# Performance work log

Hardware: AMD Instinct MI355X
Metric: run time of the kernel (lower is better)

## Reference

```python
import jax, jax.numpy as jnp
import numpy as np


def setup_inputs() -> dict:
    key = jax.random.key(0)
    k1, k2, k3 = jax.random.split(key, 3)
    B, C, H, W = 64, 256, 32, 32   # batch, hidden_dim, latent grid
    D, K = 128, 1024               # latent_dim, num_embeddings
    z = jax.random.normal(k1, (B, C, H, W), dtype=jnp.float32)
    proj_w = jax.random.normal(k2, (D, C), dtype=jnp.float32) * 0.02  # 1x1 conv kernel [out,in]
    proj_b = jnp.zeros((D,), jnp.float32)
    # codebook init uniform(-1/K, 1/K) as in torch module
    embed = (jax.random.uniform(k3, (K, D), dtype=jnp.float32) * 2.0 - 1.0) / K
    return {"z": z, "proj_w": proj_w, "proj_b": proj_b, "embed": embed}


def reference(z, proj_w, proj_b, embed):
    # 1x1 conv projection: [B,C,H,W] -> [B,H,W,D]  (fuses conv + permute)
    zp = jnp.einsum('bchw,dc->bhwd', z, proj_w) + proj_b
    B, H, W, D = zp.shape
    zf = zp.reshape(-1, D)                                   # [N, D], N = B*H*W
    # squared Euclidean distance to codebook: ||z||^2 - 2 z.e + ||e||^2  -> [N, K]
    dist = (jnp.sum(zf * zf, axis=1, keepdims=True)
            - 2.0 * (zf @ embed.T)
            + jnp.sum(embed * embed, axis=1))
    min_indices = jnp.argmin(dist, axis=1)                   # [N]
    z_q = embed[min_indices].reshape(B, H, W, D)             # codebook gather
    # straight-through estimator
    rep_z_q = zp + jax.lax.stop_gradient(z_q - zp)
    rep_z_q = rep_z_q.transpose(0, 3, 1, 2)                  # back to NCHW
    return rep_z_q, min_indices
```

## Files before the change

### kernel.cpp

```cpp
#include <hip/hip_runtime.h>

#define B_   64
#define C_   256
#define D_   128
#define HW_  1024
#define K_   1024
#define N_   65536
#define MARGIN_PREF 1.2e-3f

typedef __attribute__((ext_vector_type(8))) short short8;
typedef __attribute__((ext_vector_type(4))) float f32x4;

__device__ __forceinline__ unsigned short f2bf(float f) {
    unsigned u = __float_as_uint(f);
    return (unsigned short)((u + 0x7FFFu + ((u >> 16) & 1u)) >> 16);
}
__device__ __forceinline__ unsigned long long packdk(float d, int k) {
    unsigned u = __float_as_uint(d);
    u = (u & 0x80000000u) ? ~u : (u | 0x80000000u);
    return ((unsigned long long)u << 10) | (unsigned)k;
}
__device__ __forceinline__ float unpackd(unsigned long long key) {
    unsigned u = (unsigned)(key >> 10);
    u = (u & 0x80000000u) ? (u ^ 0x80000000u) : ~u;
    return __uint_as_float(u);
}
__device__ __forceinline__ unsigned long long min64(unsigned long long a, unsigned long long b) {
    return a < b ? a : b;
}

template <typename F>
__device__ __forceinline__ float np_sum128(F ld) {
#pragma clang fp contract(off)
    float r0 = ld(0), r1 = ld(1), r2 = ld(2), r3 = ld(3);
    float r4 = ld(4), r5 = ld(5), r6 = ld(6), r7 = ld(7);
#pragma unroll
    for (int i = 8; i < 128; i += 8) {
        r0 = r0 + ld(i + 0); r1 = r1 + ld(i + 1);
        r2 = r2 + ld(i + 2); r3 = r3 + ld(i + 3);
        r4 = r4 + ld(i + 4); r5 = r5 + ld(i + 5);
        r6 = r6 + ld(i + 6); r7 = r7 + ld(i + 7);
    }
    return ((r0 + r1) + (r2 + r3)) + ((r4 + r5) + (r6 + r7));
}

__global__ __launch_bounds__(256) void k0_norms(const float* __restrict__ embed,
                                                float* __restrict__ enorm,
                                                unsigned short* __restrict__ ebf) {
#pragma clang fp contract(off)
    int k = blockIdx.x * 256 + threadIdx.x;
    if (k >= K_) return;
    const float* e = embed + (size_t)k * D_;
    enorm[k] = np_sum128([&](int i) { float v = e[i]; return v * v; });
#pragma unroll 8
    for (int i = 0; i < 128; ++i) ebf[(size_t)k * 128 + i] = f2bf(e[i]);
}

__global__ __launch_bounds__(256) void k1_proj(const float* __restrict__ z,
                                               const float* __restrict__ w,
                                               const float* __restrict__ bias,
                                               float* __restrict__ zp,
                                               unsigned short* __restrict__ zbf) {
#pragma clang fp contract(off)
    __shared__ float zs[64][64];
    __shared__ float wsh[64][128];
    const int b   = blockIdx.x >> 4;
    const int hw0 = (blockIdx.x & 15) << 6;
    const int t   = threadIdx.x;
    const int hwg = (t & 7) * 8;
    const int dg  = (t >> 3) * 4;

    float acc[8][4];
#pragma unroll
    for (int i = 0; i < 8; ++i)
#pragma unroll
        for (int j = 0; j < 4; ++j) acc[i][j] = 0.f;

    for (int ct = 0; ct < C_; ct += 64) {
        __syncthreads();
#pragma unroll
        for (int i = 0; i < 16; ++i) {
            int idx = i * 256 + t;
            int cc = idx >> 6, hwl = idx & 63;
            zs[cc][hwl] = z[(((size_t)b * C_ + ct + cc) << 10) + hw0 + hwl];
        }
#pragma unroll
        for (int i = 0; i < 32; ++i) {
            int idx = i * 256 + t;
            int cc = idx >> 7, d = idx & 127;
            wsh[cc][d] = w[(size_t)d * C_ + ct + cc];
        }
        __syncthreads();
#pragma unroll 2
        for (int cc = 0; cc < 64; ++cc) {
            float4 za = *(const float4*)&zs[cc][hwg];
            float4 zb = *(const float4*)&zs[cc][hwg + 4];
            float4 wv = *(const float4*)&wsh[cc][dg];
            float zv[8]  = {za.x, za.y, za.z, za.w, zb.x, zb.y, zb.z, zb.w};
            float wva[4] = {wv.x, wv.y, wv.z, wv.w};
#pragma unroll
            for (int i = 0; i < 8; ++i)
#pragma unroll
                for (int j = 0; j < 4; ++j) {
                    float p = zv[i] * wva[j];
                    acc[i][j] = acc[i][j] + p;
                }
        }
    }
#pragma unroll
    for (int i = 0; i < 8; ++i)
#pragma unroll
        for (int j = 0; j < 4; ++j) {
            float v = acc[i][j] + bias[dg + j];
            size_t off = (((size_t)b * HW_ + hw0 + hwg + i) << 7) + dg + j;
            zp[off]  = v;
            zbf[off] = f2bf(v);
        }
}

__global__ __launch_bounds__(256) void k0z_znorm(const float* __restrict__ zp,
                                                 float* __restrict__ znorm) {
#pragma clang fp contract(off)
    __shared__ float zl[64][129];
    const int t = threadIdx.x, n0 = blockIdx.x * 64;
#pragma unroll
    for (int i = 0; i < 32; ++i) {
        int idx = i * 256 + t;
        zl[idx >> 7][idx & 127] = zp[(size_t)n0 * 128 + idx];
    }
    __syncthreads();
    if (t < 64)
        znorm[n0 + t] = np_sum128([&](int i) { float v = zl[t][i]; return v * v; });
}

__global__ __launch_bounds__(256) void k2_argmin(const unsigned short* __restrict__ zbf,
                                                 const unsigned short* __restrict__ ebf,
                                                 const float* __restrict__ zp,
                                                 const float* __restrict__ embed,
                                                 const float* __restrict__ enorm,
                                                 const float* __restrict__ znorm,
                                                 int* __restrict__ bestk_ws,
                                                 float* __restrict__ out_idx) {
    __shared__ unsigned char etile[16 * 272];
    const int t   = threadIdx.x;
    const int l   = t & 63;
    const int wid = t >> 6;
    const int r0  = blockIdx.x * 128 + wid * 32;
    const int lr  = l & 15;
    const int lh  = l >> 4;

    short8 zfrag[2][4];
#pragma unroll
    for (int rt = 0; rt < 2; ++rt)
#pragma unroll
        for (int dt = 0; dt < 4; ++dt)
            zfrag[rt][dt] = *(const short8*)(zbf + (((size_t)(r0 + rt * 16 + lr)) << 7) + dt * 32 + lh * 8);

    const int srow = t >> 4, scol = t & 15;

    unsigned long long bk0 = ~0ull, bk1 = ~0ull;
#pragma unroll 1
    for (int kt = 0; kt < 64; ++kt) {
        __syncthreads();
        *(short8*)(etile + srow * 272 + scol * 16) =
            *(const short8*)(ebf + (((size_t)(kt * 16 + srow)) << 7) + scol * 8);
        __syncthreads();
        short8 af[4];
#pragma unroll
        for (int dt = 0; dt < 4; ++dt)
            af[dt] = *(const short8*)(etile + lr * 272 + dt * 64 + lh * 16);
        f32x4 en4 = *(const f32x4*)(enorm + kt * 16 + lh * 4);
#pragma unroll
        for (int rt = 0; rt < 2; ++rt) {
            f32x4 acc = {0.f, 0.f, 0.f, 0.f};
#pragma unroll
            for (int dt = 0; dt < 4; ++dt)
                acc = __builtin_amdgcn_mfma_f32_16x16x32_bf16(af[dt], zfrag[rt][dt], acc, 0, 0, 0);
#pragma unroll
            for (int reg = 0; reg < 4; ++reg) {
                float dist = fmaf(-2.f, acc[reg], en4[reg]);
                int kk = kt * 16 + lh * 4 + reg;
                unsigned long long key = packdk(dist, kk);
                if (rt == 0) bk0 = min64(bk0, key); else bk1 = min64(bk1, key);
            }
        }
    }
    {
        unsigned long long o;
        o = __shfl_xor(bk0, 16, 64); bk0 = min64(bk0, o);
        o = __shfl_xor(bk0, 32, 64); bk0 = min64(bk0, o);
        o = __shfl_xor(bk1, 16, 64); bk1 = min64(bk1, o);
        o = __shfl_xor(bk1, 32, 64); bk1 = min64(bk1, o);
    }
    const float thr0 = unpackd(bk0) + MARGIN_PREF;
    const float thr1 = unpackd(bk1) + MARGIN_PREF;

    unsigned long long ca0 = 0, cb0 = 0, ca1 = 0, cb1 = 0;
    int cnt0 = 0, cnt1 = 0;
#pragma unroll 1
    for (int kt = 0; kt < 64; ++kt) {
        __syncthreads();
        *(short8*)(etile + srow * 272 + scol * 16) =
            *(const short8*)(ebf + (((size_t)(kt * 16 + srow)) << 7) + scol * 8);
        __syncthreads();
        short8 af[4];
#pragma unroll
        for (int dt = 0; dt < 4; ++dt)
            af[dt] = *(const short8*)(etile + lr * 272 + dt * 64 + lh * 16);
        f32x4 en4 = *(const f32x4*)(enorm + kt * 16 + lh * 4);
#pragma unroll
        for (int rt = 0; rt < 2; ++rt) {
            f32x4 acc = {0.f, 0.f, 0.f, 0.f};
#pragma unroll
            for (int dt = 0; dt < 4; ++dt)
                acc = __builtin_amdgcn_mfma_f32_16x16x32_bf16(af[dt], zfrag[rt][dt], acc, 0, 0, 0);
#pragma unroll
            for (int reg = 0; reg < 4; ++reg) {
                float dist = fmaf(-2.f, acc[reg], en4[reg]);
                int kk = kt * 16 + lh * 4 + reg;
                if (rt == 0) {
                    if (dist < thr0) {
                        if (cnt0 < 6)       ca0 |= (unsigned long long)kk << (10 * cnt0);
                        else if (cnt0 < 12) cb0 |= (unsigned long long)kk << (10 * (cnt0 - 6));
                        ++cnt0;
                    }
                } else {
                    if (dist < thr1) {
                        if (cnt1 < 6)       ca1 |= (unsigned long long)kk << (10 * cnt1);
                        else if (cnt1 < 12) cb1 |= (unsigned long long)kk << (10 * (cnt1 - 6));
                        ++cnt1;
                    }
                }
            }
        }
    }

    unsigned long long fin[2];
#pragma unroll
    for (int rt = 0; rt < 2; ++rt) {
        const int myrow = r0 + rt * 16 + lr;
        const float* zrow = zp + (size_t)myrow * 128;
        const float  zn   = znorm[myrow];
        unsigned long long best = ~0ull;
        unsigned long long ca = rt == 0 ? ca0 : ca1, cb = rt == 0 ? cb0 : cb1;
        int cnt = rt == 0 ? cnt0 : cnt1;

        auto refine = [&](int kk) {
#pragma clang fp contract(off)
            const float* e = embed + ((size_t)kk << 7);
            float s = 0.f;
#pragma unroll 1
            for (int d = 0; d < 128; ++d) s = fmaf(zrow[d], e[d], s);
            float T  = 2.0f * s;
            float A  = zn - T;
            float Bv = A + enorm[kk];
            best = min64(best, packdk(Bv, kk));
        };

        if (cnt <= 12) {
#pragma unroll
            for (int i = 0; i < 6; ++i)
                if (i < cnt) refine((int)((ca >> (10 * i)) & 1023ull));
#pragma unroll
            for (int i = 6; i < 12; ++i)
                if (i < cnt) refine((int)((cb >> (10 * (i - 6))) & 1023ull));
        } else {
#pragma unroll 1
            for (int kt = 0; kt < 64; ++kt)
#pragma unroll
                for (int reg = 0; reg < 4; ++reg) refine(kt * 16 + lh * 4 + reg);
        }
        unsigned long long o;
        o = __shfl_xor(best, 16, 64); best = min64(best, o);
        o = __shfl_xor(best, 32, 64); best = min64(best, o);
        fin[rt] = best;
    }

    if (l < 16) {
#pragma unroll
        for (int rt = 0; rt < 2; ++rt) {
            int row = r0 + rt * 16 + l;
            int kk  = (int)(fin[rt] & 1023ull);
            bestk_ws[row] = kk;
            out_idx[row]  = (float)kk;
        }
    }
}

__global__ __launch_bounds__(256) void k3_gather(const float* __restrict__ embed,
                                                 const int* __restrict__ bestk,
                                                 float* __restrict__ out0) {
    __shared__ float tile[64][129];
    const int b   = blockIdx.x >> 4;
    const int hw0 = (blockIdx.x & 15) << 6;
    const int t   = threadIdx.x;
    const int n0  = b * HW_ + hw0;
#pragma unroll
    for (int i = 0; i < 32; ++i) {
        int idx = i * 256 + t;
        int hwl = idx >> 7, d = idx & 127;
        int k = bestk[n0 + hwl];
        tile[hwl][d] = embed[(size_t)k * 128 + d];
    }
    __syncthreads();
#pragma unroll
    for (int i = 0; i < 32; ++i) {
        int idx = i * 256 + t;
        int d = idx >> 6, hwl = idx & 63;
        out0[(((size_t)b * D_ + d) << 10) + hw0 + hwl] = tile[hwl][d];
    }
}

extern "C" void kernel_launch(void* const* d_in, const int* in_sizes, int n_in,
                              void* d_out, int out_size, void* d_ws, size_t ws_size,
                              hipStream_t stream) {
    const float* z     = (const float*)d_in[0];
    const float* pw    = (const float*)d_in[1];
    const float* pb    = (const float*)d_in[2];
    const float* embed = (const float*)d_in[3];

    float* out0 = (float*)d_out;
    float* out1 = (float*)d_out + (size_t)B_ * D_ * HW_;

    char* ws = (char*)d_ws;
    float*          zp    = (float*)ws;
    unsigned short* zbf   = (unsigned short*)(ws + (32u << 20));
    unsigned short* ebf   = (unsigned short*)(ws + (48u << 20));
    float*          enorm = (float*)(ws + (48u << 20) + (256u << 10));
    float*          znorm = (float*)(ws + (49u << 20));
    int*            bestk = (int*)  (ws + (50u << 20));

    hipLaunchKernelGGL(k0_norms,  dim3(4),    dim3(256), 0, stream, embed, enorm, ebf);
    hipLaunchKernelGGL(k1_proj,   dim3(1024), dim3(256), 0, stream, z, pw, pb, zp, zbf);
    hipLaunchKernelGGL(k0z_znorm, dim3(1024), dim3(256), 0, stream, zp, znorm);
    hipLaunchKernelGGL(k2_argmin, dim3(512),  dim3(256), 0, stream,
                       zbf, ebf, zp, embed, enorm, znorm, bestk, out1);
    hipLaunchKernelGGL(k3_gather, dim3(1024), dim3(256), 0, stream, embed, bestk, out0);
}
```

Measured before the change: 408.4 us.

## Double-buffer swizzled codebook tiles via async global-to-LDS loads in argmin

The codebook bf16 buffer is now written in an XOR-swizzled layout so LDS fragment reads avoid bank conflicts. The argmin kernel stages 64-row codebook tiles with global_load_lds into a double buffer and prefetches the next tile while computing the current one, so there is one barrier per tile instead of two per 16 rows. Codebook norms are cached in LDS, and the first pass tracks a float minimum instead of packed 64-bit keys. LDS use rises to about 36KB per block, which may lower occupancy.

```diff
diff --git a/kernel.cpp b/kernel.cpp
--- a/kernel.cpp
+++ b/kernel.cpp
@@ -52,8 +52,15 @@
     if (k >= K_) return;
     const float* e = embed + (size_t)k * D_;
     enorm[k] = np_sum128([&](int i) { float v = e[i]; return v * v; });
-#pragma unroll 8
-    for (int i = 0; i < 128; ++i) ebf[(size_t)k * 128 + i] = f2bf(e[i]);
+    const int sw = (k & 7) << 4;
+    char* rowp = (char*)ebf + ((size_t)k << 8);
+#pragma unroll
+    for (int j = 0; j < 16; ++j) {
+        short8 v;
+#pragma unroll
+        for (int q = 0; q < 8; ++q) v[q] = (short)f2bf(e[j * 8 + q]);
+        *(short8*)(rowp + ((j * 16) ^ sw)) = v;
+    }
 }
 
 __global__ __launch_bounds__(256) void k1_proj(const float* __restrict__ z,
@@ -141,7 +148,8 @@
                                                  const float* __restrict__ znorm,
                                                  int* __restrict__ bestk_ws,
                                                  float* __restrict__ out_idx) {
-    __shared__ unsigned char etile[16 * 272];
+    __shared__ unsigned char etile[2][64 * 256];
+    __shared__ float els[1024];
     const int t   = threadIdx.x;
     const int l   = t & 63;
     const int wid = t >> 6;
@@ -156,80 +164,103 @@
         for (int dt = 0; dt < 4; ++dt)
             zfrag[rt][dt] = *(const short8*)(zbf + (((size_t)(r0 + rt * 16 + lr)) << 7) + dt * 32 + lh * 8);
 
-    const int srow = t >> 4, scol = t & 15;
-
-    unsigned long long bk0 = ~0ull, bk1 = ~0ull;
+    const int swz = (lr & 7) << 4;
+    int roff[4];
+#pragma unroll
+    for (int dt = 0; dt < 4; ++dt)
+        roff[dt] = lr * 256 + ((dt * 64 + lh * 16) ^ swz);
+
+    const char* ebf_b = (const char*)ebf;
+    auto STAGE = [&](int st, int b) {
+#pragma unroll
+        for (int j = 0; j < 4; ++j) {
+            int off = j * 4096 + (t << 4);
+            __builtin_amdgcn_global_load_lds(
+                (const __attribute__((address_space(1))) void*)(ebf_b + ((size_t)st << 14) + off),
+                (__attribute__((address_space(3))) void*)(&etile[b][off]),
+                16, 0, 0);
+        }
+    };
+
+#pragma unroll
+    for (int i = 0; i < 4; ++i) els[i * 256 + t] = enorm[i * 256 + t];
+
+    float bmin0 = 1e30f, bmin1 = 1e30f;
+    STAGE(0, 0);
 #pragma unroll 1
-    for (int kt = 0; kt < 64; ++kt) {
+    for (int st = 0; st < 16; ++st) {
         __syncthreads();
-        *(short8*)(etile + srow * 272 + scol * 16) =
-            *(const short8*)(ebf + (((size_t)(kt * 16 + srow)) << 7) + scol * 8);
-        __syncthreads();
-        short8 af[4];
-#pragma unroll
-        for (int dt = 0; dt < 4; ++dt)
-            af[dt] = *(const short8*)(etile + lr * 272 + dt * 64 + lh * 16);
-        f32x4 en4 = *(const f32x4*)(enorm + kt * 16 + lh * 4);
-#pragma unroll
-        for (int rt = 0; rt < 2; ++rt) {
-            f32x4 acc = {0.f, 0.f, 0.f, 0.f};
-#pragma unroll
-            for (int dt = 0; dt < 4; ++dt)
-                acc = __builtin_amdgcn_mfma_f32_16x16x32_bf16(af[dt], zfrag[rt][dt], acc, 0, 0, 0);
+        if (st < 15) STAGE(st + 1, (st + 1) & 1);
+        const unsigned char* buf = etile[st & 1];
+#pragma unroll
+        for (int kf = 0; kf < 4; ++kf) {
+            short8 af[4];
+#pragma unroll
+            for (int dt = 0; dt < 4; ++dt)
+                af[dt] = *(const short8*)(buf + kf * 4096 + roff[dt]);
+            f32x4 en4 = *(const f32x4*)(els + st * 64 + kf * 16 + lh * 4);
+            f32x4 a0 = {0.f, 0.f, 0.f, 0.f};
+            f32x4 a1 = {0.f, 0.f, 0.f, 0.f};
+#pragma unroll
+            for (int dt = 0; dt < 4; ++dt)
+                a0 = __builtin_amdgcn_mfma_f32_16x16x32_bf16(af[dt], zfrag[0][dt], a0, 0, 0, 0);
+#pragma unroll
+            for (int dt = 0; dt < 4; ++dt)
+                a1 = __builtin_amdgcn_mfma_f32_16x16x32_bf16(af[dt], zfrag[1][dt], a1, 0, 0, 0);
 #pragma unroll
             for (int reg = 0; reg < 4; ++reg) {
-                float dist = fmaf(-2.f, acc[reg], en4[reg]);
-                int kk = kt * 16 + lh * 4 + reg;
-                unsigned long long key = packdk(dist, kk);
-                if (rt == 0) bk0 = min64(bk0, key); else bk1 = min64(bk1, key);
+                bmin0 = fminf(bmin0, fmaf(-2.f, a0[reg], en4[reg]));
+                bmin1 = fminf(bmin1, fmaf(-2.f, a1[reg], en4[reg]));
             }
         }
     }
     {
-        unsigned long long o;
-        o = __shfl_xor(bk0, 16, 64); bk0 = min64(bk0, o);
-        o = __shfl_xor(bk0, 32, 64); bk0 = min64(bk0, o);
-        o = __shfl_xor(bk1, 16, 64); bk1 = min64(bk1, o);
-        o = __shfl_xor(bk1, 32, 64); bk1 = min64(bk1, o);
-    }
-    const float thr0 = unpackd(bk0) + MARGIN_PREF;
-    const float thr1 = unpackd(bk1) + MARGIN_PREF;
+        bmin0 = fminf(bmin0, __shfl_xor(bmin0, 16, 64));
+        bmin0 = fminf(bmin0, __shfl_xor(bmin0, 32, 64));
+        bmin1 = fminf(bmin1, __shfl_xor(bmin1, 16, 64));
+        bmin1 = fminf(bmin1, __shfl_xor(bmin1, 32, 64));
+    }
+    const float thr0 = bmin0 + MARGIN_PREF;
+    const float thr1 = bmin1 + MARGIN_PREF;
 
     unsigned long long ca0 = 0, cb0 = 0, ca1 = 0, cb1 = 0;
     int cnt0 = 0, cnt1 = 0;
+    __syncthreads();
+    STAGE(0, 0);
 #pragma unroll 1
-    for (int kt = 0; kt < 64; ++kt) {
+    for (int st = 0; st < 16; ++st) {
         __syncthreads();
-        *(short8*)(etile + srow * 272 + scol * 16) =
-            *(const short8*)(ebf + (((size_t)(kt * 16 + srow)) << 7) + scol * 8);
-        __syncthreads();
-        short8 af[4];
-#pragma unroll
-        for (int dt = 0; dt < 4; ++dt)
-            af[dt] = *(const short8*)(etile + lr * 272 + dt * 64 + lh * 16);
-        f32x4 en4 = *(const f32x4*)(enorm + kt * 16 + lh * 4);
-#pragma unroll
-        for (int rt = 0; rt < 2; ++rt) {
-            f32x4 acc = {0.f, 0.f, 0.f, 0.f};
-#pragma unroll
-            for (int dt = 0; dt < 4; ++dt)
-                acc = __builtin_amdgcn_mfma_f32_16x16x32_bf16(af[dt], zfrag[rt][dt], acc, 0, 0, 0);
+        if (st < 15) STAGE(st + 1, (st + 1) & 1);
+        const unsigned char* buf = etile[st & 1];
+#pragma unroll
+        for (int kf = 0; kf < 4; ++kf) {
+            short8 af[4];
+#pragma unroll
+            for (int dt = 0; dt < 4; ++dt)
+                af[dt] = *(const short8*)(buf + kf * 4096 + roff[dt]);
+            f32x4 en4 = *(const f32x4*)(els + st * 64 + kf * 16 + lh * 4);
+            f32x4 a0 = {0.f, 0.f, 0.f, 0.f};
+            f32x4 a1 = {0.f, 0.f, 0.f, 0.f};
+#pragma unroll
+            for (int dt = 0; dt < 4; ++dt)
+                a0 = __builtin_amdgcn_mfma_f32_16x16x32_bf16(af[dt], zfrag[0][dt], a0, 0, 0, 0);
+#pragma unroll
+            for (int dt = 0; dt < 4; ++dt)
+                a1 = __builtin_amdgcn_mfma_f32_16x16x32_bf16(af[dt], zfrag[1][dt], a1, 0, 0, 0);
 #pragma unroll
             for (int reg = 0; reg < 4; ++reg) {
-                float dist = fmaf(-2.f, acc[reg], en4[reg]);
-                int kk = kt * 16 + lh * 4 + reg;
-                if (rt == 0) {
-                    if (dist < thr0) {
-                        if (cnt0 < 6)       ca0 |= (unsigned long long)kk << (10 * cnt0);
-                        else if (cnt0 < 12) cb0 |= (unsigned long long)kk << (10 * (cnt0 - 6));
-                        ++cnt0;
-                    }
-                } else {
-                    if (dist < thr1) {
-                        if (cnt1 < 6)       ca1 |= (unsigned long long)kk << (10 * cnt1);
-                        else if (cnt1 < 12) cb1 |= (unsigned long long)kk << (10 * (cnt1 - 6));
-                        ++cnt1;
-                    }
+                int kk = st * 64 + kf * 16 + lh * 4 + reg;
+                float d0 = fmaf(-2.f, a0[reg], en4[reg]);
+                if (d0 < thr0) {
+                    if (cnt0 < 6)       ca0 |= (unsigned long long)kk << (10 * cnt0);
+                    else if (cnt0 < 12) cb0 |= (unsigned long long)kk << (10 * (cnt0 - 6));
+                    ++cnt0;
+                }
+                float d1 = fmaf(-2.f, a1[reg], en4[reg]);
+                if (d1 < thr1) {
+                    if (cnt1 < 6)       ca1 |= (unsigned long long)kk << (10 * cnt1);
+                    else if (cnt1 < 12) cb1 |= (unsigned long long)kk << (10 * (cnt1 - 6));
+                    ++cnt1;
                 }
             }
         }
@@ -239,7 +270,7 @@
 #pragma unroll
     for (int rt = 0; rt < 2; ++rt) {
         const int myrow = r0 + rt * 16 + lr;
-        const float* zrow = zp + (size_t)myrow * 128;
+        const float* zrow = zp + ((size_t)myrow << 7);
         const float  zn   = znorm[myrow];
         unsigned long long best = ~0ull;
         unsigned long long ca = rt == 0 ? ca0 : ca1, cb = rt == 0 ? cb0 : cb1;
@@ -266,9 +297,12 @@
                 if (i < cnt) refine((int)((cb >> (10 * (i - 6))) & 1023ull));
         } else {
 #pragma unroll 1
-            for (int kt = 0; kt < 64; ++kt)
-#pragma unroll
-                for (int reg = 0; reg < 4; ++reg) refine(kt * 16 + lh * 4 + reg);
+            for (int st = 0; st < 16; ++st)
+#pragma unroll
+                for (int kf = 0; kf < 4; ++kf)
+#pragma unroll
+                    for (int reg = 0; reg < 4; ++reg)
+                        refine(st * 64 + kf * 16 + lh * 4 + reg);
         }
         unsigned long long o;
         o = __shfl_xor(best, 16, 64); best = min64(best, o);
```

Measured after the change: 369.5 us. -9.5%, faster.
